# Kernel tuning notes

Hardware: AMD Instinct MI355X
Metric: run time of the kernel (lower is better)

Reference implementation:

```python
import jax, jax.numpy as jnp
import numpy as np
from jax import lax

# static config matching init_kwargs
H, W = 128, 128
THETA_RES, RHO_RES = 1.0, 1.0
C_IN, C_OUT = 64, 64
A = int(np.round(180.0 / THETA_RES))            # num angle bins = 180
R = int(np.ceil(np.sqrt(H * H + W * W) / RHO_RES))  # num rho bins = 182


def _make_rho_idx():
    # rho bin index for every (angle, pixel); pixels flattened h-major (h*W + w)
    th = np.arange(A, dtype=np.float64) * THETA_RES * np.pi / 180.0
    hh, ww = np.meshgrid(np.arange(H), np.arange(W), indexing='ij')
    xs = (ww - W / 2.0).ravel()
    ys = (hh - H / 2.0).ravel()
    r = np.round((xs[None, :] * np.cos(th)[:, None]
                  + ys[None, :] * np.sin(th)[:, None]) / RHO_RES).astype(np.int32)
    r = r + R // 2
    return np.clip(r, 0, R - 1)  # [A, H*W] int32


def dht(x, rho_idx):
    # Hough scatter: [N,C,H,W] -> [N,C,A,R]
    N, C, h, w = x.shape
    xf = x.reshape(N * C, h * w).T  # [HW, NC]

    def step(_, idx_a):
        acc = jax.ops.segment_sum(xf, idx_a, num_segments=R)  # [R, NC]
        return None, acc

    _, ht = lax.scan(step, None, rho_idx)       # [A, R, NC]
    return ht.transpose(2, 0, 1).reshape(N, C, A, R)


def idht(ht, rho_idx):
    # inverse Hough gather (transpose of dht): [N,C,A,R] -> [N,C,H,W]
    N, C, a, r = ht.shape
    hf = ht.reshape(N * C, a, r).transpose(1, 0, 2)  # [A, NC, R]

    def step(acc, args):
        ht_a, idx_a = args
        return acc + ht_a[:, idx_a], None  # gather along rho -> [NC, HW]

    acc0 = jnp.zeros((N * C, H * W), ht.dtype)
    acc, _ = lax.scan(step, acc0, (hf, rho_idx))
    return acc.reshape(N, C, H, W)


def conv91_relu(x, w, b, groups):
    # Conv2d kernel (9,1), padding (4,0), stride 1 + ReLU
    y = lax.conv_general_dilated(x, w, (1, 1), [(4, 4), (0, 0)],
                                 dimension_numbers=('NCHW', 'OIHW', 'NCHW'),
                                 feature_group_count=groups)
    return jax.nn.relu(y + b[None, :, None, None])


def setup_inputs():
    key = jax.random.key(0)
    ks = jax.random.split(key, 7)
    N = 4
    x = jax.random.normal(ks[0], (N, C_IN, H, W), dtype=jnp.float32)
    s1 = 1.0 / np.sqrt(9.0)
    s2 = 1.0 / np.sqrt(9.0 * C_IN)
    w1 = jax.random.normal(ks[1], (C_IN, 1, 9, 1), jnp.float32) * s1
    b1 = jax.random.normal(ks[2], (C_IN,), jnp.float32) * 0.01
    w2 = jax.random.normal(ks[3], (C_IN, C_IN, 9, 1), jnp.float32) * s2
    b2 = jax.random.normal(ks[4], (C_IN,), jnp.float32) * 0.01
    w3 = jax.random.normal(ks[5], (C_OUT, C_IN, 9, 1), jnp.float32) * s2
    b3 = jax.random.normal(ks[6], (C_OUT,), jnp.float32) * 0.01
    rho_idx = jnp.asarray(_make_rho_idx())  # [A, H*W] int32, precomputed buffer
    return {"x": x, "rho_idx": rho_idx, "w1": w1, "b1": b1,
            "w2": w2, "b2": b2, "w3": w3, "b3": b3}


def reference(x, rho_idx, w1, b1, w2, b2, w3, b3):
    out = dht(x, rho_idx)                       # [N,C,A,R]
    out = conv91_relu(out, w1, b1, groups=C_IN) # grouped (9,1) conv
    out = conv91_relu(out, w2, b2, groups=1)
    out = conv91_relu(out, w3, b3, groups=1)
    return idht(out, rho_idx)                   # [N,C_OUT,H,W]
```

## Files before the change

kernel.cpp:

```cpp
#include <hip/hip_runtime.h>

typedef unsigned short ushort_t;
typedef __attribute__((ext_vector_type(8))) short short8;
typedef __attribute__((ext_vector_type(4))) float float4v;
typedef __attribute__((ext_vector_type(2))) float float2v;

#define HW 16384
#define A_BINS 180
#define R_BINS 182
#define AP 188
#define CCH 64
#define NB 4
#define NC 256
#define MROWS (A_BINS * R_BINS)
#define MPROWS (AP * R_BINS)
#define PADPX HW
#define PLSTRIDE 17664

static __device__ __forceinline__ float b2f(ushort_t u) {
    union { unsigned u32; float f; } c; c.u32 = ((unsigned)u) << 16; return c.f;
}
static __device__ __forceinline__ float u2f(unsigned u) {
    union { unsigned u32; float f; } c; c.u32 = u; return c.f;
}
static __device__ __forceinline__ ushort_t f2b(float f) {
    union { float f; unsigned u; } c; c.f = f;
    unsigned r = c.u + 0x7fffu + ((c.u >> 16) & 1u);
    return (ushort_t)(r >> 16);
}
static __device__ __forceinline__ void pkaccu(float2v& a, unsigned u) {
    float2v b; b.x = u2f(u << 16); b.y = u2f(u & 0xffff0000u);
    asm("v_pk_add_f32 %0, %1, %0" : "+v"(a) : "v"(b));
}

union PrepShared {
    float tile[64][65];
    struct {
        int hist[4][R_BINS];
        int tot[R_BINS];
        int offl[R_BINS + 1];
        int cur[4][R_BINS];
        ushort_t sp[PLSTRIDE];
    } c;
};

__global__ __launch_bounds__(256) void k_prep(const float* __restrict__ x,
                                              ushort_t* __restrict__ xT,
                                              ushort_t* __restrict__ ht0,
                                              ushort_t* __restrict__ bufA,
                                              ushort_t* __restrict__ bufB,
                                              const float* __restrict__ w2,
                                              const float* __restrict__ w3,
                                              ushort_t* __restrict__ w2b,
                                              ushort_t* __restrict__ w3b,
                                              const int* __restrict__ rho,
                                              int* __restrict__ offs,
                                              ushort_t* __restrict__ plist) {
    __shared__ PrepShared u;
    int blk = blockIdx.x, t = threadIdx.x;
    if (blk < 1024) {
        int lane = t & 63, g = t >> 6;
        int pBase = (blk & 255) * 64;
        int ncBase = (blk >> 8) * 64;
#pragma unroll
        for (int i = 0; i < 16; ++i) {
            int ncl = g + i * 4;
            u.tile[ncl][lane] = x[(size_t)(ncBase + ncl) * HW + pBase + lane];
        }
        __syncthreads();
#pragma unroll
        for (int i = 0; i < 16; ++i) {
            int pl = g + i * 4;
            xT[(size_t)(pBase + pl) * 256 + ncBase + lane] = f2b(u.tile[lane][pl]);
        }
        return;
    }
    if (blk < 1337) {
        int sblk = blk - 1024;
        if (sblk == 312) {
            if (t < 64) ((uint2*)(xT + (size_t)PADPX * NC))[t] = (uint2){0u, 0u};
            return;
        }
        if (sblk < 24) {
            int b = sblk >> 3, j = sblk & 7;
            int ap = (j < 4) ? j : (184 + (j - 4));
            ushort_t* base = (b == 0 ? ht0 : (b == 1 ? bufA : bufB));
            uint4* p = (uint4*)(base + (size_t)ap * (R_BINS * NC));
            int n16 = R_BINS * NC / 8;
            for (int i = t; i < n16; i += 256) p[i] = (uint4){0, 0, 0, 0};
            return;
        }
        int rep = sblk - 24;
        const float* w = (rep >= 144) ? w3 : w2;
        ushort_t* wb = (rep >= 144) ? w3b : w2b;
        int idx = (rep % 144) * 256 + t;
        int j = idx & 7;
        int lane = (idx >> 3) & 63;
        int cot = (idx >> 9) & 3;
        int h = (idx >> 11) & 1;
        int k = idx >> 12;
        int co = cot * 16 + (lane & 15);
        int ci = h * 32 + (lane >> 4) * 8 + j;
        wb[idx] = f2b(w[(co * 64 + ci) * 9 + k]);
        return;
    }
    int a = blk - 1337, lane = t & 63, wv = t >> 6;
    for (int i = t; i < 4 * R_BINS; i += 256) ((int*)u.c.hist)[i] = 0;
    __syncthreads();
    const int* rA = rho + (size_t)a * HW;
#pragma unroll 4
    for (int i = 0; i < 64; ++i) {
        int r = rA[t + i * 256];
        atomicAdd(&u.c.hist[wv][r], 1);
    }
    __syncthreads();
    if (t < R_BINS) u.c.tot[t] = u.c.hist[0][t] + u.c.hist[1][t] + u.c.hist[2][t] + u.c.hist[3][t];
    __syncthreads();
    if (wv == 0) {
        int b0 = lane * 3;
        int c0 = (b0     < R_BINS) ? ((u.c.tot[b0]     + 7) & ~7) : 0;
        int c1 = (b0 + 1 < R_BINS) ? ((u.c.tot[b0 + 1] + 7) & ~7) : 0;
        int c2 = (b0 + 2 < R_BINS) ? ((u.c.tot[b0 + 2] + 7) & ~7) : 0;
        int sum = c0 + c1 + c2, inc = sum;
#pragma unroll
        for (int d = 1; d < 64; d <<= 1) {
            int vv = __shfl_up(inc, d);
            if (lane >= d) inc += vv;
        }
        int excl = inc - sum;
        if (b0     < R_BINS) u.c.offl[b0]     = excl;
        if (b0 + 1 < R_BINS) u.c.offl[b0 + 1] = excl + c0;
        if (b0 + 2 < R_BINS) u.c.offl[b0 + 2] = excl + c0 + c1;
        if (lane == 63) u.c.offl[R_BINS] = inc;
    }
    __syncthreads();
    if (t < R_BINS) {
        int b = u.c.offl[t];
        u.c.cur[0][t] = b; b += u.c.hist[0][t];
        u.c.cur[1][t] = b; b += u.c.hist[1][t];
        u.c.cur[2][t] = b; b += u.c.hist[2][t];
        u.c.cur[3][t] = b;
    }
    if (t <= R_BINS) offs[a * (R_BINS + 1) + t] = u.c.offl[t];
    __syncthreads();
#pragma unroll 4
    for (int i = 0; i < 64; ++i) {
        int p = t + i * 256;
        int r = rA[p];
        int pos = atomicAdd(&u.c.cur[wv][r], 1);
        u.c.sp[pos] = (ushort_t)p;
    }
    __syncthreads();
    if (t < R_BINS) {
        int base = u.c.offl[t] + u.c.tot[t];
        int pend = u.c.offl[t + 1];
        for (int k = base; k < pend; ++k) u.c.sp[k] = (ushort_t)PADPX;
    }
    __syncthreads();
    int len = u.c.offl[R_BINS];
    const uint4* spv = (const uint4*)u.c.sp;
    uint4* plv = (uint4*)(plist + (size_t)a * PLSTRIDE);
    for (int i = t; i < len / 8; i += 256) plv[i] = spv[i];
}

__global__ __launch_bounds__(256, 4) void k_dht_g7(const ushort_t* __restrict__ xT,
                                                   const int* __restrict__ offs,
                                                   const ushort_t* __restrict__ plist,
                                                   ushort_t* __restrict__ ht0) {
    int ax = blockIdx.x;
    int a = ax >> 1, half = ax & 1;
    int part = blockIdx.y;
    int t = threadIdx.x, lane = t & 63, wv = t >> 6;
    int wslot = part * 4 + wv;
    int nl = lane & 15;
    unsigned lhb = (unsigned)nl * 16;
    unsigned shsel = (lane & 16) ? 16u : 0u;
    const char* xh = (const char*)xT + half * 256;
    const uint4* plq = (const uint4*)(plist + (size_t)a * PLSTRIDE);
    const int* offA = offs + a * (R_BINS + 1);
    size_t obase = (size_t)(a + 4) * (R_BINS * NC) + half * 128;
    for (int r = wslot; r < R_BINS; r += 64) {
        int off = __builtin_amdgcn_readfirstlane(offA[r]);
        int end = __builtin_amdgcn_readfirstlane(offA[r + 1]);
        float2v ac0 = (float2v){0.f, 0.f}, ac1 = (float2v){0.f, 0.f};
        float2v ac2 = (float2v){0.f, 0.f}, ac3 = (float2v){0.f, 0.f};
        int j = off;
        if (j < end) {
            uint4 w = plq[j >> 3];
            for (;;) {
                int jn = j + 8;
                uint4 wn = (uint4){0u, 0u, 0u, 0u};
                bool more = jn < end;
                if (more) wn = plq[jn >> 3];
                {
                    unsigned we = (lane & 32) ? w.y : w.x;
                    unsigned ps = (we >> shsel) & 0xffffu;
                    uint4 u = *(const uint4*)(xh + ((size_t)ps << 9) + lhb);
                    pkaccu(ac0, u.x); pkaccu(ac1, u.y);
                    pkaccu(ac2, u.z); pkaccu(ac3, u.w);
                }
                {
                    unsigned we = (lane & 32) ? w.w : w.z;
                    unsigned ps = (we >> shsel) & 0xffffu;
                    uint4 u = *(const uint4*)(xh + ((size_t)ps << 9) + lhb);
                    pkaccu(ac0, u.x); pkaccu(ac1, u.y);
                    pkaccu(ac2, u.z); pkaccu(ac3, u.w);
                }
                if (!more) break;
                w = wn; j = jn;
            }
        }
        float rs[8] = {ac0.x, ac0.y, ac1.x, ac1.y, ac2.x, ac2.y, ac3.x, ac3.y};
#pragma unroll
        for (int c = 0; c < 8; ++c) {
            rs[c] += __shfl_xor(rs[c], 16);
            rs[c] += __shfl_xor(rs[c], 32);
        }
        if (lane < 16) {
            uint4 o;
            o.x = (unsigned)f2b(rs[0]) | ((unsigned)f2b(rs[1]) << 16);
            o.y = (unsigned)f2b(rs[2]) | ((unsigned)f2b(rs[3]) << 16);
            o.z = (unsigned)f2b(rs[4]) | ((unsigned)f2b(rs[5]) << 16);
            o.w = (unsigned)f2b(rs[6]) | ((unsigned)f2b(rs[7]) << 16);
            *(uint4*)(ht0 + obase + (size_t)r * NC + nl * 8) = o;
        }
    }
}

__global__ __launch_bounds__(256) void k_conv1(const ushort_t* __restrict__ ht0,
                                               const float* __restrict__ w1,
                                               const float* __restrict__ b1,
                                               ushort_t* __restrict__ bufA) {
    int t = threadIdx.x, c = t & 63;
    int r = blockIdx.x;
    int a0 = blockIdx.y * 30;
    float wr[9];
#pragma unroll
    for (int k = 0; k < 9; ++k) wr[k] = w1[c * 9 + k];
    float bb = b1[c];
    const ushort_t* ip = ht0 + ((size_t)a0 * R_BINS + r) * NC + t;
    float v[38];
#pragma unroll
    for (int j = 0; j < 38; ++j) v[j] = b2f(ip[(size_t)j * (R_BINS * NC)]);
    ushort_t* op = bufA + ((size_t)(a0 + 4) * R_BINS + r) * NC + t;
#pragma unroll
    for (int i = 0; i < 30; ++i) {
        float s = bb;
#pragma unroll
        for (int k = 0; k < 9; ++k) s = fmaf(v[i + k], wr[k], s);
        op[(size_t)i * (R_BINS * NC)] = f2b(fmaxf(s, 0.f));
    }
}

__global__ __launch_bounds__(256) void k_gemm(const ushort_t* __restrict__ in,
                                              const ushort_t* __restrict__ wb,
                                              const float* __restrict__ bias,
                                              ushort_t* __restrict__ out,
                                              int outRowOff) {
    __shared__ ushort_t Bs[36864];
    int t = threadIdx.x, lane = t & 63, wv = t >> 6;
    {
        const uint4* src = (const uint4*)wb;
        uint4* dst = (uint4*)Bs;
        for (int i = t; i < 36864 / 8; i += 256) dst[i] = src[i];
    }
    __syncthreads();
    int m = lane & 15, q = lane >> 4;
    int n = blockIdx.y;
    int rowBase = blockIdx.x * 256 + wv * 64;
    const ushort_t* inN = in + n * 64;
    size_t rof[4];
#pragma unroll
    for (int tl = 0; tl < 4; ++tl) {
        int row = rowBase + tl * 16 + m;
        int rowc = row < MROWS ? row : (MROWS - 1);
        rof[tl] = (size_t)rowc * NC;
    }
    float4v acc[4][4];
#pragma unroll
    for (int tl = 0; tl < 4; ++tl)
#pragma unroll
        for (int i = 0; i < 4; ++i) acc[tl][i] = (float4v){0.f, 0.f, 0.f, 0.f};

#pragma unroll
    for (int k = 0; k < 9; ++k) {
#pragma unroll
        for (int h = 0; h < 2; ++h) {
            const ushort_t* base = inN + (size_t)k * (R_BINS * NC) + h * 32 + q * 8;
            short8 af0 = *(const short8*)(base + rof[0]);
            short8 af1 = *(const short8*)(base + rof[1]);
            short8 af2 = *(const short8*)(base + rof[2]);
            short8 af3 = *(const short8*)(base + rof[3]);
            const ushort_t* bl = Bs + (size_t)((k * 2 + h) * 4) * 512 + lane * 8;
            short8 b0 = *(const short8*)(bl);
            short8 b1v = *(const short8*)(bl + 512);
            short8 b2v = *(const short8*)(bl + 1024);
            short8 b3v = *(const short8*)(bl + 1536);
            acc[0][0] = __builtin_amdgcn_mfma_f32_16x16x32_bf16(af0, b0, acc[0][0], 0, 0, 0);
            acc[0][1] = __builtin_amdgcn_mfma_f32_16x16x32_bf16(af0, b1v, acc[0][1], 0, 0, 0);
            acc[0][2] = __builtin_amdgcn_mfma_f32_16x16x32_bf16(af0, b2v, acc[0][2], 0, 0, 0);
            acc[0][3] = __builtin_amdgcn_mfma_f32_16x16x32_bf16(af0, b3v, acc[0][3], 0, 0, 0);
            acc[1][0] = __builtin_amdgcn_mfma_f32_16x16x32_bf16(af1, b0, acc[1][0], 0, 0, 0);
            acc[1][1] = __builtin_amdgcn_mfma_f32_16x16x32_bf16(af1, b1v, acc[1][1], 0, 0, 0);
            acc[1][2] = __builtin_amdgcn_mfma_f32_16x16x32_bf16(af1, b2v, acc[1][2], 0, 0, 0);
            acc[1][3] = __builtin_amdgcn_mfma_f32_16x16x32_bf16(af1, b3v, acc[1][3], 0, 0, 0);
            acc[2][0] = __builtin_amdgcn_mfma_f32_16x16x32_bf16(af2, b0, acc[2][0], 0, 0, 0);
            acc[2][1] = __builtin_amdgcn_mfma_f32_16x16x32_bf16(af2, b1v, acc[2][1], 0, 0, 0);
            acc[2][2] = __builtin_amdgcn_mfma_f32_16x16x32_bf16(af2, b2v, acc[2][2], 0, 0, 0);
            acc[2][3] = __builtin_amdgcn_mfma_f32_16x16x32_bf16(af2, b3v, acc[2][3], 0, 0, 0);
            acc[3][0] = __builtin_amdgcn_mfma_f32_16x16x32_bf16(af3, b0, acc[3][0], 0, 0, 0);
            acc[3][1] = __builtin_amdgcn_mfma_f32_16x16x32_bf16(af3, b1v, acc[3][1], 0, 0, 0);
            acc[3][2] = __builtin_amdgcn_mfma_f32_16x16x32_bf16(af3, b2v, acc[3][2], 0, 0, 0);
            acc[3][3] = __builtin_amdgcn_mfma_f32_16x16x32_bf16(af3, b3v, acc[3][3], 0, 0, 0);
        }
    }

    ushort_t* outN = out + n * 64;
#pragma unroll
    for (int tl = 0; tl < 4; ++tl) {
#pragma unroll
        for (int cot = 0; cot < 4; ++cot) {
            int co = cot * 16 + m;
            float bv = bias[co];
#pragma unroll
            for (int i = 0; i < 4; ++i) {
                int rowD = rowBase + tl * 16 + q * 4 + i;
                float v = fmaxf(acc[tl][cot][i] + bv, 0.f);
                if (rowD < MROWS) outN[(size_t)(rowD + outRowOff) * NC + co] = f2b(v);
            }
        }
    }
}

union SharedIdht {
    int rhoL[A_BINS * 32];
    float tile[2 * 256 * 33];
};

#define IDHT_LOAD(S, ang) do { \
    int4 rv0_ = *(const int4*)&u.rhoL[(ang) * 32 + wq * 8]; \
    int4 rv1_ = *(const int4*)&u.rhoL[(ang) * 32 + wq * 8 + 4]; \
    const char* bA_ = (const char*)buf3 + (size_t)(ang) * (R_BINS * NC * 2); \
    { unsigned r_ = (unsigned)(h ? rv0_.y : rv0_.x); S[0] = *(const uint4*)(bA_ + ((size_t)r_ << 9) + lhb); } \
    { unsigned r_ = (unsigned)(h ? rv0_.w : rv0_.z); S[1] = *(const uint4*)(bA_ + ((size_t)r_ << 9) + lhb); } \
    { unsigned r_ = (unsigned)(h ? rv1_.y : rv1_.x); S[2] = *(const uint4*)(bA_ + ((size_t)r_ << 9) + lhb); } \
    { unsigned r_ = (unsigned)(h ? rv1_.w : rv1_.z); S[3] = *(const uint4*)(bA_ + ((size_t)r_ << 9) + lhb); } \
    } while (0)

#define IDHT_CONSUME(S) do { \
    _Pragma("unroll") \
    for (int p_ = 0; p_ < 4; ++p_) { \
        pkaccu(accp[4 * p_ + 0], S[p_].x); \
        pkaccu(accp[4 * p_ + 1], S[p_].y); \
        pkaccu(accp[4 * p_ + 2], S[p_].z); \
        pkaccu(accp[4 * p_ + 3], S[p_].w); \
    } } while (0)

__global__ __launch_bounds__(512, 2) void k_idht(const ushort_t* __restrict__ buf3,
                                                 const int* __restrict__ rho,
                                                 float* __restrict__ outp) {
    __shared__ SharedIdht u;
    int t = threadIdx.x, lane = t & 63, wv = t >> 6;
    int grp = wv >> 2;
    int wq = wv & 3;
    int P0 = blockIdx.x * 32;
    int h = lane >> 5;
    unsigned lhb = (unsigned)(lane & 31) * 16;
    for (int i = t; i < A_BINS * 32; i += 512) {
        int a = i >> 5, px = i & 31;
        u.rhoL[a * 32 + px] = rho[(size_t)a * HW + P0 + px];
    }
    __syncthreads();
    float2v accp[16];
#pragma unroll
    for (int i = 0; i < 16; ++i) accp[i] = (float2v){0.f, 0.f};
    int a0 = grp * 90;

    uint4 S0[4], S1[4], S2[4];
    IDHT_LOAD(S0, a0);
    IDHT_LOAD(S1, a0 + 1);
    IDHT_LOAD(S2, a0 + 2);
    for (int k = 0; k <= 84; k += 3) {
        IDHT_CONSUME(S0); IDHT_LOAD(S0, a0 + k + 3);
        IDHT_CONSUME(S1); IDHT_LOAD(S1, a0 + k + 4);
        IDHT_CONSUME(S2); IDHT_LOAD(S2, a0 + k + 5);
    }
    IDHT_CONSUME(S0);
    IDHT_CONSUME(S1);
    IDHT_CONSUME(S2);

    __syncthreads();
#pragma unroll
    for (int p = 0; p < 4; ++p) {
        int px = wq * 8 + p * 2 + h;
#pragma unroll
        for (int cc = 0; cc < 8; ++cc)
            u.tile[(size_t)grp * 8448 + ((lane & 31) * 8 + cc) * 33 + px] =
                accp[4 * p + (cc >> 1)][cc & 1];
    }
    __syncthreads();
    int px = t & 31, nc0 = t >> 5;
    float* on = outp + P0 + px;
#pragma unroll
    for (int k = 0; k < 16; ++k) {
        int nc = nc0 + k * 16;
        on[(size_t)nc * HW] = u.tile[nc * 33 + px] + u.tile[8448 + nc * 33 + px];
    }
}

extern "C" void kernel_launch(void* const* d_in, const int* in_sizes, int n_in,
                              void* d_out, int out_size, void* d_ws, size_t ws_size,
                              hipStream_t stream) {
    const float* x   = (const float*)d_in[0];
    const int*   rho = (const int*)d_in[1];
    const float* w1  = (const float*)d_in[2];
    const float* b1  = (const float*)d_in[3];
    const float* w2  = (const float*)d_in[4];
    const float* b2  = (const float*)d_in[5];
    const float* w3  = (const float*)d_in[6];
    const float* b3  = (const float*)d_in[7];
    float* outp = (float*)d_out;

    char* ws = (char*)d_ws;
    size_t off = 0;
    auto alloc = [&](size_t bytes) -> void* {
        void* p = ws + off;
        off = (off + bytes + 255) & ~(size_t)255;
        return p;
    };
    ushort_t* xT    = (ushort_t*)alloc((size_t)(HW + 8) * NC * 2);
    ushort_t* ht0   = (ushort_t*)alloc((size_t)AP * R_BINS * NC * 2);
    ushort_t* bufA  = (ushort_t*)alloc((size_t)AP * R_BINS * NC * 2);
    ushort_t* bufB  = (ushort_t*)alloc((size_t)AP * R_BINS * NC * 2);
    ushort_t* buf3  = (ushort_t*)alloc((size_t)A_BINS * R_BINS * NC * 2);
    ushort_t* w2b   = (ushort_t*)alloc(36864 * 2);
    ushort_t* w3b   = (ushort_t*)alloc(36864 * 2);
    int*      offs  = (int*)alloc((size_t)A_BINS * (R_BINS + 1) * 4);
    ushort_t* plist = (ushort_t*)alloc((size_t)A_BINS * PLSTRIDE * 2);

    k_prep<<<1517, 256, 0, stream>>>(x, xT, ht0, bufA, bufB, w2, w3, w2b, w3b,
                                     rho, offs, plist);
    k_dht_g7<<<dim3(360, 16), 256, 0, stream>>>(xT, offs, plist, ht0);
    k_conv1<<<dim3(R_BINS, 6), 256, 0, stream>>>(ht0, w1, b1, bufA);
    k_gemm<<<dim3(128, NB), 256, 0, stream>>>(bufA, w2b, b2, bufB, 728);
    k_gemm<<<dim3(128, NB), 256, 0, stream>>>(bufB, w3b, b3, buf3, 0);
    k_idht<<<dim3(512), 512, 0, stream>>>(buf3, rho, outp);
}
```

Measured before the change: 316.4 us.

## Stage contiguous rho-row window per angle in LDS for iDHT gather

```diff
diff --git a/kernel.cpp b/kernel.cpp
--- a/kernel.cpp
+++ b/kernel.cpp
@@ -333,78 +333,88 @@
 }
 
 union SharedIdht {
-    int rhoL[A_BINS * 32];
-    float tile[2 * 256 * 33];
+    struct {
+        int rhoL[A_BINS * 32];
+        ushort_t st[2][34 * 256];
+    } s;
+    float tile[256 * 33];
 };
-
-#define IDHT_LOAD(S, ang) do { \
-    int4 rv0_ = *(const int4*)&u.rhoL[(ang) * 32 + wq * 8]; \
-    int4 rv1_ = *(const int4*)&u.rhoL[(ang) * 32 + wq * 8 + 4]; \
-    const char* bA_ = (const char*)buf3 + (size_t)(ang) * (R_BINS * NC * 2); \
-    { unsigned r_ = (unsigned)(h ? rv0_.y : rv0_.x); S[0] = *(const uint4*)(bA_ + ((size_t)r_ << 9) + lhb); } \
-    { unsigned r_ = (unsigned)(h ? rv0_.w : rv0_.z); S[1] = *(const uint4*)(bA_ + ((size_t)r_ << 9) + lhb); } \
-    { unsigned r_ = (unsigned)(h ? rv1_.y : rv1_.x); S[2] = *(const uint4*)(bA_ + ((size_t)r_ << 9) + lhb); } \
-    { unsigned r_ = (unsigned)(h ? rv1_.w : rv1_.z); S[3] = *(const uint4*)(bA_ + ((size_t)r_ << 9) + lhb); } \
-    } while (0)
-
-#define IDHT_CONSUME(S) do { \
-    _Pragma("unroll") \
-    for (int p_ = 0; p_ < 4; ++p_) { \
-        pkaccu(accp[4 * p_ + 0], S[p_].x); \
-        pkaccu(accp[4 * p_ + 1], S[p_].y); \
-        pkaccu(accp[4 * p_ + 2], S[p_].z); \
-        pkaccu(accp[4 * p_ + 3], S[p_].w); \
-    } } while (0)
 
 __global__ __launch_bounds__(512, 2) void k_idht(const ushort_t* __restrict__ buf3,
                                                  const int* __restrict__ rho,
                                                  float* __restrict__ outp) {
     __shared__ SharedIdht u;
-    int t = threadIdx.x, lane = t & 63, wv = t >> 6;
-    int grp = wv >> 2;
-    int wq = wv & 3;
+    int t = threadIdx.x;
     int P0 = blockIdx.x * 32;
-    int h = lane >> 5;
-    unsigned lhb = (unsigned)(lane & 31) * 16;
+    int px = t >> 4;
+    int ncg = t & 15;
     for (int i = t; i < A_BINS * 32; i += 512) {
-        int a = i >> 5, px = i & 31;
-        u.rhoL[a * 32 + px] = rho[(size_t)a * HW + P0 + px];
-    }
-    __syncthreads();
-    float2v accp[16];
-#pragma unroll
-    for (int i = 0; i < 16; ++i) accp[i] = (float2v){0.f, 0.f};
-    int a0 = grp * 90;
-
-    uint4 S0[4], S1[4], S2[4];
-    IDHT_LOAD(S0, a0);
-    IDHT_LOAD(S1, a0 + 1);
-    IDHT_LOAD(S2, a0 + 2);
-    for (int k = 0; k <= 84; k += 3) {
-        IDHT_CONSUME(S0); IDHT_LOAD(S0, a0 + k + 3);
-        IDHT_CONSUME(S1); IDHT_LOAD(S1, a0 + k + 4);
-        IDHT_CONSUME(S2); IDHT_LOAD(S2, a0 + k + 5);
-    }
-    IDHT_CONSUME(S0);
-    IDHT_CONSUME(S1);
-    IDHT_CONSUME(S2);
-
-    __syncthreads();
-#pragma unroll
-    for (int p = 0; p < 4; ++p) {
-        int px = wq * 8 + p * 2 + h;
-#pragma unroll
-        for (int cc = 0; cc < 8; ++cc)
-            u.tile[(size_t)grp * 8448 + ((lane & 31) * 8 + cc) * 33 + px] =
-                accp[4 * p + (cc >> 1)][cc & 1];
-    }
-    __syncthreads();
-    int px = t & 31, nc0 = t >> 5;
-    float* on = outp + P0 + px;
+        int a = i >> 5, p = i & 31;
+        u.s.rhoL[i] = rho[(size_t)a * HW + P0 + p];
+    }
+    __syncthreads();
+    float2v acc[8];
+#pragma unroll
+    for (int i = 0; i < 8; ++i) acc[i] = (float2v){0.f, 0.f};
+    {
+        int r0 = u.s.rhoL[0], r1 = u.s.rhoL[31];
+        int rmin0 = r0 < r1 ? r0 : r1;
+        int cnt0 = (r0 < r1 ? r1 - r0 : r0 - r1) + 1;
+        const uint4* src = (const uint4*)(buf3 + (size_t)rmin0 * NC);
+        uint4* dst = (uint4*)u.s.st[0];
+        for (int i = t; i < cnt0 * 32; i += 512) dst[i] = src[i];
+    }
+    __syncthreads();
+
+    for (int a = 0; a < A_BINS; ++a) {
+        int cur = a & 1;
+        uint4 pv0, pv1, pv2;
+        bool g0 = false, g1 = false, g2 = false;
+        if (a + 1 < A_BINS) {
+            int r0 = u.s.rhoL[(a + 1) * 32], r1 = u.s.rhoL[(a + 1) * 32 + 31];
+            int rminN = r0 < r1 ? r0 : r1;
+            int lim = ((r0 < r1 ? r1 - r0 : r0 - r1) + 1) * 32;
+            const uint4* src = (const uint4*)(buf3 + (size_t)(a + 1) * (R_BINS * NC)
+                                              + (size_t)rminN * NC);
+            g0 = t < lim; g1 = t + 512 < lim; g2 = t + 1024 < lim;
+            if (g0) pv0 = src[t];
+            if (g1) pv1 = src[t + 512];
+            if (g2) pv2 = src[t + 1024];
+        }
+        {
+            int r0 = u.s.rhoL[a * 32], r1 = u.s.rhoL[a * 32 + 31];
+            int rmin = r0 < r1 ? r0 : r1;
+            int row = u.s.rhoL[a * 32 + px] - rmin;
+            const uint4* sp = (const uint4*)(u.s.st[cur] + row * 256 + ncg * 16);
+            uint4 v0 = sp[0];
+            uint4 v1 = sp[1];
+            pkaccu(acc[0], v0.x); pkaccu(acc[1], v0.y);
+            pkaccu(acc[2], v0.z); pkaccu(acc[3], v0.w);
+            pkaccu(acc[4], v1.x); pkaccu(acc[5], v1.y);
+            pkaccu(acc[6], v1.z); pkaccu(acc[7], v1.w);
+        }
+        if (a + 1 < A_BINS) {
+            uint4* dst = (uint4*)u.s.st[cur ^ 1];
+            if (g0) dst[t] = pv0;
+            if (g1) dst[t + 512] = pv1;
+            if (g2) dst[t + 1024] = pv2;
+        }
+        __syncthreads();
+    }
+
+#pragma unroll
+    for (int k = 0; k < 8; ++k) {
+        int nc = ncg * 16 + 2 * k;
+        u.tile[nc * 33 + px] = acc[k].x;
+        u.tile[(nc + 1) * 33 + px] = acc[k].y;
+    }
+    __syncthreads();
+    int px2 = t & 31, nc0 = t >> 5;
+    float* on = outp + P0 + px2;
 #pragma unroll
     for (int k = 0; k < 16; ++k) {
         int nc = nc0 + k * 16;
-        on[(size_t)nc * HW] = u.tile[nc * 33 + px] + u.tile[8448 + nc * 33 + px];
+        on[(size_t)nc * HW] = u.tile[nc * 33 + px2];
     }
 }
 
```

Measured after the change: 374.7 us. +18.4%, slower.
